# Optimization experiments

Hardware: AMD Instinct MI355X
Metric: run time of the kernel (lower is better)

Reference implementation:

```python
import jax, jax.numpy as jnp
import numpy as np

SIZE = 32000
PAD_IDX = 0
SMOOTHING = 0.1
CONFIDENCE = 1.0 - SMOOTHING
NUM_EXPERTS = 8
LOAD_COEF = 0.01
Z_COEF = 0.001
NORMALIZE_LENGTH = True


def setup_inputs() -> dict:
    key = jax.random.key(0)
    k0, k1, k2, k3, k4 = jax.random.split(key, 5)
    B, S, K = 2, 2048, 2
    return {
        "x": jax.random.normal(k0, (B, S, SIZE), dtype=jnp.float32),
        "topk_values": jax.random.uniform(k1, (B, S, K), dtype=jnp.float32),
        "gate_logits": jax.random.normal(k2, (B, S, NUM_EXPERTS), dtype=jnp.float32),
        "target": jax.random.randint(k3, (B, S), 0, SIZE, dtype=jnp.int64),
        "topk_indices": jax.random.randint(k4, (B, S, K), 0, NUM_EXPERTS, dtype=jnp.int64),
    }


def reference(x, topk_values, gate_logits, target, topk_indices):
    # ---- label smoothing KLDiv ----
    xf = x.reshape(-1, SIZE)            # [N, V]
    t = target.reshape(-1)              # [N]
    N = xf.shape[0]
    ignore = t == PAD_IDX               # [N]
    total = N - ignore.sum()
    t0 = jnp.where(ignore, 0, t)
    smooth_val = SMOOTHING / (SIZE - 1)
    # true_dist built under torch.no_grad -> constant
    true_dist = jnp.full((N, SIZE), smooth_val, dtype=xf.dtype)
    true_dist = true_dist.at[jnp.arange(N), t0].set(CONFIDENCE)
    true_dist = jax.lax.stop_gradient(true_dist)
    logp = jax.nn.log_softmax(xf, axis=1)
    # KLDivLoss(reduction='none'): target * (log(target) - input)
    kl = true_dist * (jnp.log(true_dist) - logp)
    kl = jnp.where(ignore[:, None], jnp.zeros((), xf.dtype), kl)
    denom = total.astype(xf.dtype) if NORMALIZE_LENGTH else jnp.asarray(x.shape[0], xf.dtype)
    label_smoothing_loss = kl.sum() / denom

    # ---- load balancing loss (fused histogram instead of per-expert loop) ----
    # torch version uses .item() per expert -> fully detached from autodiff
    flat_idx = topk_indices.reshape(-1)
    expert_loads = jnp.zeros(NUM_EXPERTS, xf.dtype).at[flat_idx].add(1.0)
    logits_sum = jnp.zeros(NUM_EXPERTS, xf.dtype).at[flat_idx].add(topk_values.reshape(-1))
    num_elements = topk_indices.shape[0] * topk_indices.shape[1]
    load_loss = jax.lax.stop_gradient(
        (NUM_EXPERTS / num_elements) * (expert_loads * logits_sum).sum()
    )

    # ---- router z-loss ----
    router_z_loss = jnp.mean(jnp.square(jax.nn.logsumexp(gate_logits, axis=-1)))

    return label_smoothing_loss + LOAD_COEF * load_loss + Z_COEF * router_z_loss
```

## Files before the change

kernel.cpp:

```cpp
#include <hip/hip_runtime.h>
#include <hip/hip_bf16.h>
#include <math.h>

#define SIZE_V 32000
#define NROWS  4096
#define NEXP   8
#define NTOPK  8192
#define RBLK   320

__device__ inline float waveReduceSum(float v) {
#pragma unroll
    for (int off = 32; off; off >>= 1) v += __shfl_xor(v, off, 64);
    return v;
}

__global__ __launch_bounds__(RBLK) void row_kernel(const float* __restrict__ x,
                                                   const int* __restrict__ target,
                                                   const float* __restrict__ gate,
                                                   float* __restrict__ klrow,
                                                   float* __restrict__ zrow,
                                                   float self_ent, float smooth) {
    __shared__ float smS[5];
    __shared__ float smX[5];

    const int row = blockIdx.x;
    const int tid = threadIdx.x;
    const float4* xr = (const float4*)(x + (size_t)row * SIZE_V);

    int t = 0;
    float xt = 0.f;
    float4 ga = {0, 0, 0, 0}, gb = {0, 0, 0, 0};
    if (tid == 0) {
        t  = target[row];
        xt = x[(size_t)row * SIZE_V + t];
        const float4* gr = (const float4*)(gate + (size_t)row * NEXP);
        ga = gr[0];
        gb = gr[1];
    }

    float sAcc[5] = {0, 0, 0, 0, 0};
    float xAcc[5] = {0, 0, 0, 0, 0};
    for (int j = 0; j < 5; ++j) {
#pragma unroll
        for (int u = 0; u < 5; ++u) {
            float4 v = xr[tid + (j * 5 + u) * RBLK];
            sAcc[u] += (__expf(v.x) + __expf(v.y)) + (__expf(v.z) + __expf(v.w));
            xAcc[u] += (v.x + v.y) + (v.z + v.w);
        }
    }
    float s  = ((sAcc[0] + sAcc[1]) + (sAcc[2] + sAcc[3])) + sAcc[4];
    float sx = ((xAcc[0] + xAcc[1]) + (xAcc[2] + xAcc[3])) + xAcc[4];

    const int lane = tid & 63, wid = tid >> 6;
    float ws_ = waveReduceSum(s);
    float wsx = waveReduceSum(sx);
    if (lane == 0) { smS[wid] = ws_; smX[wid] = wsx; }
    __syncthreads();

    if (tid == 0) {
        float S  = ((smS[0] + smS[1]) + (smS[2] + smS[3])) + smS[4];
        float SX = ((smX[0] + smX[1]) + (smX[2] + smX[3])) + smX[4];
        float logZ = __logf(S);
        float kl = 0.f;
        if (t != 0) {
            float sum_logp = SX - (float)SIZE_V * logZ;
            float logp_t = xt - logZ;
            kl = self_ent - (smooth * (sum_logp - logp_t) + 0.9f * logp_t);
        }
        klrow[row] = kl;

        float mx = fmaxf(fmaxf(fmaxf(ga.x, ga.y), fmaxf(ga.z, ga.w)),
                         fmaxf(fmaxf(gb.x, gb.y), fmaxf(gb.z, gb.w)));
        float se = __expf(ga.x - mx) + __expf(ga.y - mx) + __expf(ga.z - mx) + __expf(ga.w - mx)
                 + __expf(gb.x - mx) + __expf(gb.y - mx) + __expf(gb.z - mx) + __expf(gb.w - mx);
        float lse = mx + __logf(se);
        zrow[row] = lse * lse;
    }
}

__global__ __launch_bounds__(1024) void tail_kernel(const float* __restrict__ klrow,
                                                    const float* __restrict__ zrow,
                                                    const int* __restrict__ target,
                                                    const int* __restrict__ tidx,
                                                    const float* __restrict__ tval,
                                                    float* __restrict__ out) {
    __shared__ float sm[16][20];
    const int tid = threadIdx.x;

    float4 kv = ((const float4*)klrow)[tid];
    float4 zv = ((const float4*)zrow)[tid];
    int4   tv = ((const int4*)target)[tid];
    float kacc = (kv.x + kv.y) + (kv.z + kv.w);
    float zacc = (zv.x + zv.y) + (zv.z + zv.w);
    float cacc = ((tv.x != 0) ? 1.f : 0.f) + ((tv.y != 0) ? 1.f : 0.f)
               + ((tv.z != 0) ? 1.f : 0.f) + ((tv.w != 0) ? 1.f : 0.f);

    const int4*   ti4 = (const int4*)tidx;
    const float4* tv4 = (const float4*)tval;
    int4   e0 = ti4[tid * 2], e1 = ti4[tid * 2 + 1];
    float4 v0 = tv4[tid * 2], v1 = tv4[tid * 2 + 1];
    int   ee[8] = {e0.x, e0.y, e0.z, e0.w, e1.x, e1.y, e1.z, e1.w};
    float vv[8] = {v0.x, v0.y, v0.z, v0.w, v1.x, v1.y, v1.z, v1.w};

    float cnt[NEXP]  = {0, 0, 0, 0, 0, 0, 0, 0};
    float vsum[NEXP] = {0, 0, 0, 0, 0, 0, 0, 0};
#pragma unroll
    for (int i = 0; i < 8; i++) {
#pragma unroll
        for (int k = 0; k < NEXP; k++) {
            bool hit = (ee[i] == k);
            cnt[k]  += hit ? 1.f : 0.f;
            vsum[k] += hit ? vv[i] : 0.f;
        }
    }

    kacc = waveReduceSum(kacc);
    cacc = waveReduceSum(cacc);
    zacc = waveReduceSum(zacc);
#pragma unroll
    for (int k = 0; k < NEXP; k++) {
        cnt[k]  = waveReduceSum(cnt[k]);
        vsum[k] = waveReduceSum(vsum[k]);
    }

    const int lane = tid & 63, wid = tid >> 6;
    if (lane == 0) {
        sm[wid][0] = kacc;
        sm[wid][1] = cacc;
        sm[wid][2] = zacc;
#pragma unroll
        for (int k = 0; k < NEXP; k++) {
            sm[wid][3 + k]  = cnt[k];
            sm[wid][11 + k] = vsum[k];
        }
    }
    __syncthreads();

    if (tid == 0) {
        float KL = 0.f, TOT = 0.f, Z = 0.f;
        float C[NEXP] = {0, 0, 0, 0, 0, 0, 0, 0};
        float V[NEXP] = {0, 0, 0, 0, 0, 0, 0, 0};
        for (int w = 0; w < 16; w++) {
            KL += sm[w][0];
            TOT += sm[w][1];
            Z  += sm[w][2];
#pragma unroll
            for (int k = 0; k < NEXP; k++) {
                C[k] += sm[w][3 + k];
                V[k] += sm[w][11 + k];
            }
        }
        float dot = 0.f;
#pragma unroll
        for (int k = 0; k < NEXP; k++) dot += C[k] * V[k];

        float label = KL / TOT;
        float load  = ((float)NEXP / (float)NROWS) * dot;
        float z     = Z / (float)NROWS;
        out[0] = label + 0.01f * load + 0.001f * z;
    }
}

extern "C" void kernel_launch(void* const* d_in, const int* in_sizes, int n_in,
                              void* d_out, int out_size, void* d_ws, size_t ws_size,
                              hipStream_t stream) {
    const float* x      = (const float*)d_in[0];
    const float* tval   = (const float*)d_in[1];
    const float* gate   = (const float*)d_in[2];
    const int*   target = (const int*)d_in[3];
    const int*   tidx   = (const int*)d_in[4];
    float* out = (float*)d_out;
    float* klrow = (float*)d_ws;
    float* zrow  = (float*)d_ws + NROWS;

    const double sv = 0.1 / (double)(SIZE_V - 1);
    const float self_ent = (float)((double)(SIZE_V - 1) * sv * log(sv) + 0.9 * log(0.9));

    hipLaunchKernelGGL(row_kernel, dim3(NROWS), dim3(RBLK), 0, stream,
                       x, target, gate, klrow, zrow, self_ent, (float)sv);
    hipLaunchKernelGGL(tail_kernel, dim3(1), dim3(1024), 0, stream,
                       klrow, zrow, target, tidx, tval, out);
}
```

Measured before the change: 104.0 us.

## Fuse tail reduction into row kernel via atomics and last-block finalization

Drops the separate single-block tail kernel. Each row block now atomically accumulates its KL term, non-pad count and z-loss into a small workspace. Block 0 also computes the expert-load histogram dot product, and the last block to finish, found through an atomic counter, writes the final scalar. The row loads of x also switch to nontemporal loads. This saves a kernel launch and the per-row workspace round trip. In exchange it adds a memset launch, contended float atomics on three addresses, and a non-deterministic summation order.

```diff
diff --git a/kernel.cpp b/kernel.cpp
--- a/kernel.cpp
+++ b/kernel.cpp
@@ -8,32 +8,39 @@
 #define NTOPK  8192
 #define RBLK   320
 
+typedef float floatx4 __attribute__((ext_vector_type(4)));
+
+
 __device__ inline float waveReduceSum(float v) {
 #pragma unroll
     for (int off = 32; off; off >>= 1) v += __shfl_xor(v, off, 64);
     return v;
 }
 
-__global__ __launch_bounds__(RBLK) void row_kernel(const float* __restrict__ x,
-                                                   const int* __restrict__ target,
-                                                   const float* __restrict__ gate,
-                                                   float* __restrict__ klrow,
-                                                   float* __restrict__ zrow,
-                                                   float self_ent, float smooth) {
+__global__ __launch_bounds__(RBLK) void fused_kernel(const float* __restrict__ x,
+                                                     const int* __restrict__ target,
+                                                     const float* __restrict__ gate,
+                                                     const int* __restrict__ tidx,
+                                                     const float* __restrict__ tval,
+                                                     float* __restrict__ ws,
+                                                     float* __restrict__ out,
+                                                     float self_ent, float smooth) {
     __shared__ float smS[5];
     __shared__ float smX[5];
+    __shared__ float smB[5][16];
 
     const int row = blockIdx.x;
     const int tid = threadIdx.x;
-    const float4* xr = (const float4*)(x + (size_t)row * SIZE_V);
+    const int lane = tid & 63, wid = tid >> 6;
+    const floatx4* xr = (const floatx4*)(x + (size_t)row * SIZE_V);
 
     int t = 0;
     float xt = 0.f;
-    float4 ga = {0, 0, 0, 0}, gb = {0, 0, 0, 0};
+    floatx4 ga = {0, 0, 0, 0}, gb = {0, 0, 0, 0};
     if (tid == 0) {
         t  = target[row];
         xt = x[(size_t)row * SIZE_V + t];
-        const float4* gr = (const float4*)(gate + (size_t)row * NEXP);
+        const floatx4* gr = (const floatx4*)(gate + (size_t)row * NEXP);
         ga = gr[0];
         gb = gr[1];
     }
@@ -43,7 +50,7 @@
     for (int j = 0; j < 5; ++j) {
 #pragma unroll
         for (int u = 0; u < 5; ++u) {
-            float4 v = xr[tid + (j * 5 + u) * RBLK];
+            floatx4 v = __builtin_nontemporal_load(xr + tid + (j * 5 + u) * RBLK);
             sAcc[u] += (__expf(v.x) + __expf(v.y)) + (__expf(v.z) + __expf(v.w));
             xAcc[u] += (v.x + v.y) + (v.z + v.w);
         }
@@ -51,10 +58,9 @@
     float s  = ((sAcc[0] + sAcc[1]) + (sAcc[2] + sAcc[3])) + sAcc[4];
     float sx = ((xAcc[0] + xAcc[1]) + (xAcc[2] + xAcc[3])) + xAcc[4];
 
-    const int lane = tid & 63, wid = tid >> 6;
-    float ws_ = waveReduceSum(s);
-    float wsx = waveReduceSum(sx);
-    if (lane == 0) { smS[wid] = ws_; smX[wid] = wsx; }
+    s  = waveReduceSum(s);
+    sx = waveReduceSum(sx);
+    if (lane == 0) { smS[wid] = s; smX[wid] = sx; }
     __syncthreads();
 
     if (tid == 0) {
@@ -67,97 +73,75 @@
             float logp_t = xt - logZ;
             kl = self_ent - (smooth * (sum_logp - logp_t) + 0.9f * logp_t);
         }
-        klrow[row] = kl;
-
         float mx = fmaxf(fmaxf(fmaxf(ga.x, ga.y), fmaxf(ga.z, ga.w)),
                          fmaxf(fmaxf(gb.x, gb.y), fmaxf(gb.z, gb.w)));
         float se = __expf(ga.x - mx) + __expf(ga.y - mx) + __expf(ga.z - mx) + __expf(ga.w - mx)
                  + __expf(gb.x - mx) + __expf(gb.y - mx) + __expf(gb.z - mx) + __expf(gb.w - mx);
         float lse = mx + __logf(se);
-        zrow[row] = lse * lse;
+
+        atomicAdd(ws + 0, kl);
+        atomicAdd(ws + 1, (t != 0) ? 1.f : 0.f);
+        atomicAdd(ws + 2, lse * lse);
     }
-}
 
-__global__ __launch_bounds__(1024) void tail_kernel(const float* __restrict__ klrow,
-                                                    const float* __restrict__ zrow,
-                                                    const int* __restrict__ target,
-                                                    const int* __restrict__ tidx,
-                                                    const float* __restrict__ tval,
-                                                    float* __restrict__ out) {
-    __shared__ float sm[16][20];
-    const int tid = threadIdx.x;
-
-    float4 kv = ((const float4*)klrow)[tid];
-    float4 zv = ((const float4*)zrow)[tid];
-    int4   tv = ((const int4*)target)[tid];
-    float kacc = (kv.x + kv.y) + (kv.z + kv.w);
-    float zacc = (zv.x + zv.y) + (zv.z + zv.w);
-    float cacc = ((tv.x != 0) ? 1.f : 0.f) + ((tv.y != 0) ? 1.f : 0.f)
-               + ((tv.z != 0) ? 1.f : 0.f) + ((tv.w != 0) ? 1.f : 0.f);
-
-    const int4*   ti4 = (const int4*)tidx;
-    const float4* tv4 = (const float4*)tval;
-    int4   e0 = ti4[tid * 2], e1 = ti4[tid * 2 + 1];
-    float4 v0 = tv4[tid * 2], v1 = tv4[tid * 2 + 1];
-    int   ee[8] = {e0.x, e0.y, e0.z, e0.w, e1.x, e1.y, e1.z, e1.w};
-    float vv[8] = {v0.x, v0.y, v0.z, v0.w, v1.x, v1.y, v1.z, v1.w};
-
-    float cnt[NEXP]  = {0, 0, 0, 0, 0, 0, 0, 0};
-    float vsum[NEXP] = {0, 0, 0, 0, 0, 0, 0, 0};
+    if (row == 0) {
+        const int4*   ti4 = (const int4*)tidx;
+        const float4* tv4 = (const float4*)tval;
+        float cnt[NEXP]  = {0, 0, 0, 0, 0, 0, 0, 0};
+        float vsum[NEXP] = {0, 0, 0, 0, 0, 0, 0, 0};
+        for (int i = tid; i < NTOPK / 4; i += RBLK) {
+            int4   e = ti4[i];
+            float4 v = tv4[i];
+            int   ee[4] = {e.x, e.y, e.z, e.w};
+            float vv[4] = {v.x, v.y, v.z, v.w};
 #pragma unroll
-    for (int i = 0; i < 8; i++) {
+            for (int q = 0; q < 4; q++)
+#pragma unroll
+                for (int k = 0; k < NEXP; k++) {
+                    bool h = (ee[q] == k);
+                    cnt[k]  += h ? 1.f : 0.f;
+                    vsum[k] += h ? vv[q] : 0.f;
+                }
+        }
 #pragma unroll
         for (int k = 0; k < NEXP; k++) {
-            bool hit = (ee[i] == k);
-            cnt[k]  += hit ? 1.f : 0.f;
-            vsum[k] += hit ? vv[i] : 0.f;
+            cnt[k]  = waveReduceSum(cnt[k]);
+            vsum[k] = waveReduceSum(vsum[k]);
+        }
+        if (lane == 0) {
+#pragma unroll
+            for (int k = 0; k < NEXP; k++) {
+                smB[wid][k]     = cnt[k];
+                smB[wid][8 + k] = vsum[k];
+            }
+        }
+        __syncthreads();
+        if (tid == 0) {
+            float dot = 0.f;
+#pragma unroll
+            for (int k = 0; k < NEXP; k++) {
+                float C = 0.f, V = 0.f;
+                for (int w = 0; w < 5; w++) { C += smB[w][k]; V += smB[w][8 + k]; }
+                dot += C * V;
+            }
+            atomicExch(ws + 4, dot);
         }
     }
 
-    kacc = waveReduceSum(kacc);
-    cacc = waveReduceSum(cacc);
-    zacc = waveReduceSum(zacc);
-#pragma unroll
-    for (int k = 0; k < NEXP; k++) {
-        cnt[k]  = waveReduceSum(cnt[k]);
-        vsum[k] = waveReduceSum(vsum[k]);
-    }
-
-    const int lane = tid & 63, wid = tid >> 6;
-    if (lane == 0) {
-        sm[wid][0] = kacc;
-        sm[wid][1] = cacc;
-        sm[wid][2] = zacc;
-#pragma unroll
-        for (int k = 0; k < NEXP; k++) {
-            sm[wid][3 + k]  = cnt[k];
-            sm[wid][11 + k] = vsum[k];
+    if (tid == 0) {
+        __threadfence();
+        unsigned old = atomicAdd((unsigned int*)(ws + 3), 1u);
+        if (old == NROWS - 1) {
+            __threadfence();
+            float KL  = atomicAdd(ws + 0, 0.f);
+            float TOT = atomicAdd(ws + 1, 0.f);
+            float Z   = atomicAdd(ws + 2, 0.f);
+            float dot = atomicAdd(ws + 4, 0.f);
+            float label = KL / TOT;
+            float load  = ((float)NEXP / (float)NROWS) * dot;
+            float z     = Z / (float)NROWS;
+            out[0] = label + 0.01f * load + 0.001f * z;
         }
-    }
-    __syncthreads();
-
-    if (tid == 0) {
-        float KL = 0.f, TOT = 0.f, Z = 0.f;
-        float C[NEXP] = {0, 0, 0, 0, 0, 0, 0, 0};
-        float V[NEXP] = {0, 0, 0, 0, 0, 0, 0, 0};
-        for (int w = 0; w < 16; w++) {
-            KL += sm[w][0];
-            TOT += sm[w][1];
-            Z  += sm[w][2];
-#pragma unroll
-            for (int k = 0; k < NEXP; k++) {
-                C[k] += sm[w][3 + k];
-                V[k] += sm[w][11 + k];
-            }
-        }
-        float dot = 0.f;
-#pragma unroll
-        for (int k = 0; k < NEXP; k++) dot += C[k] * V[k];
-
-        float label = KL / TOT;
-        float load  = ((float)NEXP / (float)NROWS) * dot;
-        float z     = Z / (float)NROWS;
-        out[0] = label + 0.01f * load + 0.001f * z;
     }
 }
 
@@ -170,14 +154,12 @@
     const int*   target = (const int*)d_in[3];
     const int*   tidx   = (const int*)d_in[4];
     float* out = (float*)d_out;
-    float* klrow = (float*)d_ws;
-    float* zrow  = (float*)d_ws + NROWS;
+    float* ws  = (float*)d_ws;
 
     const double sv = 0.1 / (double)(SIZE_V - 1);
     const float self_ent = (float)((double)(SIZE_V - 1) * sv * log(sv) + 0.9 * log(0.9));
 
-    hipLaunchKernelGGL(row_kernel, dim3(NROWS), dim3(RBLK), 0, stream,
-                       x, target, gate, klrow, zrow, self_ent, (float)sv);
-    hipLaunchKernelGGL(tail_kernel, dim3(1), dim3(1024), 0, stream,
-                       klrow, zrow, target, tidx, tval, out);
+    (void)hipMemsetAsync(ws, 0, 16, stream);
+    hipLaunchKernelGGL(fused_kernel, dim3(NROWS), dim3(RBLK), 0, stream,
+                       x, target, gate, tidx, tval, ws, out, self_ent, (float)sv);
 }
```

Measured after the change: 292.0 us. 181% more time.
